# Performance work log

Hardware: AMD Instinct MI355X
Metric: run time of the kernel (lower is better)

The kernel has to match this reference:

```python
import jax, jax.numpy as jnp
import numpy as np

T = 1_048_576          # sequence length
NUM_INPUTS = 16        # symbol vocab for _delta table
MAX_OUTPUT = 25        # softmax width / counter range


def setup_inputs() -> dict:
    key = jax.random.key(0)
    k1, k2, k3 = jax.random.split(key, 3)
    input_seq = jax.random.randint(k1, (T,), 0, NUM_INPUTS)
    # learned params (random instead of the degenerate zero init so the
    # recurrence and softmax are non-trivial)
    delta = jax.random.normal(k2, (NUM_INPUTS,), dtype=jnp.float32) * 0.5
    out_bias = jax.random.normal(k3, (MAX_OUTPUT,), dtype=jnp.float32) * 0.1
    out_scale = jnp.ones((1,), dtype=jnp.float32)
    return {"input_seq": input_seq, "delta": delta,
            "out_bias": out_bias, "out_scale": out_scale}


def reference(input_seq, delta, out_bias, out_scale):
    max_out = out_bias.shape[0]
    # per-step increments: vectorized gather  [T]
    deltas = delta[input_seq]

    # scalar counter recurrence with clamp (non-associative -> lax.scan)
    def step(c, d):
        c = jnp.clip(c + d, 0.0, float(max_out - 1))
        return c, c

    _, counters = jax.lax.scan(step, jnp.float32(0.0), deltas)  # [T]

    # vectorized readout: distances [T, max_out] -> logits -> softmax
    positions = jnp.arange(max_out, dtype=jnp.float32)
    distances = jnp.abs(positions[None, :] - counters[:, None])
    logits = -distances * out_scale + out_bias
    return jax.nn.softmax(logits, axis=-1)  # [T, max_out]
```

## Files before the change

kernel.cpp:

```cpp
#include <hip/hip_runtime.h>

#define T_LEN   1048576
#define K1B     1024
#define BLK     256
#define SEG     256
#define NSEG    (T_LEN / SEG)
#define MAXO    25
#define CLAMP_HI 24.0f
#define BIGF    1e30f

typedef float f4v __attribute__((ext_vector_type(4)));

struct Trip { float a, l, h; };

__device__ __forceinline__ Trip comb(Trip x, Trip y) {
    Trip r;
    r.a = x.a + y.a;
    r.l = fmaxf(x.l + y.a, y.l);
    r.h = fminf(fmaxf(x.h + y.a, y.l), y.h);
    return r;
}
__device__ __forceinline__ float applyT(Trip p, float c) {
    return fminf(fmaxf(c + p.a, p.l), p.h);
}
__device__ __forceinline__ Trip shflUpTrip(Trip v, int off) {
    Trip r;
    r.a = __shfl_up(v.a, off, 64);
    r.l = __shfl_up(v.l, off, 64);
    r.h = __shfl_up(v.h, off, 64);
    return r;
}

__global__ __launch_bounds__(BLK)
void k1_fused(const int* __restrict__ seq, const float* __restrict__ delta,
              float* __restrict__ tri, float* __restrict__ entry,
              int* __restrict__ cnt) {
    __shared__ float dl[16];
    __shared__ int isLast;
    __shared__ Trip agg[4];
    const int tid = threadIdx.x, lane = tid & 63, wid = tid >> 6;
    const int bid = blockIdx.x;

    if (tid < 16) dl[tid] = delta[tid];
    __syncthreads();

    const int4 s4 = *(const int4*)(seq + bid * 1024 + tid * 4);
    Trip t = {dl[s4.x], 0.0f, CLAMP_HI};
    { Trip e = {dl[s4.y], 0.0f, CLAMP_HI}; t = comb(t, e); }
    { Trip e = {dl[s4.z], 0.0f, CLAMP_HI}; t = comb(t, e); }
    { Trip e = {dl[s4.w], 0.0f, CLAMP_HI}; t = comb(t, e); }

#pragma unroll
    for (int off = 1; off < 64; off <<= 1) {
        Trip o = shflUpTrip(t, off);
        if (lane >= off) t = comb(o, t);
    }
    if (lane == 63) {
        const int sid = bid * 4 + wid;
        tri[3 * sid + 0] = t.a;
        tri[3 * sid + 1] = t.l;
        tri[3 * sid + 2] = t.h;
    }
    __syncthreads();
    if (tid == 0) {
        __threadfence();
        isLast = (atomicAdd(cnt, 1) == K1B - 1);
    }
    __syncthreads();
    if (!isLast) return;

    __threadfence();
    f4v f[12];
    const f4v* p = (const f4v*)(tri + tid * 48);
#pragma unroll
    for (int i = 0; i < 12; ++i) f[i] = p[i];
    const float* fp = (const float*)f;

    Trip loc[16];
#pragma unroll
    for (int k = 0; k < 16; ++k)
        loc[k] = {fp[3 * k], fp[3 * k + 1], fp[3 * k + 2]};

    Trip incl = loc[0];
#pragma unroll
    for (int k = 1; k < 16; ++k) incl = comb(incl, loc[k]);

#pragma unroll
    for (int off = 1; off < 64; off <<= 1) {
        Trip o = shflUpTrip(incl, off);
        if (lane >= off) incl = comb(o, incl);
    }
    if (lane == 63) agg[wid] = incl;
    __syncthreads();

    Trip W = {0.0f, -BIGF, BIGF};
    for (int w = 0; w < wid; ++w) W = comb(W, agg[w]);
    const Trip prev = shflUpTrip(incl, 1);
    const Trip E = (lane == 0) ? W : comb(W, prev);

    float ebuf[16];
    float c = applyT(E, 0.0f);
    ebuf[0] = c;
#pragma unroll
    for (int k = 0; k < 15; ++k) { c = applyT(loc[k], c); ebuf[k + 1] = c; }

    f4v* ep = (f4v*)(entry + 16 * tid);
#pragma unroll
    for (int i = 0; i < 4; ++i)
        ep[i] = ((const f4v*)ebuf)[i];
}

__global__ __launch_bounds__(BLK)
void k2_out(const int* __restrict__ seq, const float* __restrict__ delta,
            const float* __restrict__ bias, const float* __restrict__ scale,
            const float* __restrict__ entry, float* __restrict__ out) {
    __shared__ __align__(16) float tile[SEG * MAXO];
    __shared__ Trip agg[4];
    __shared__ float dl[16], bs[MAXO];

    const int tid = threadIdx.x, lane = tid & 63, wid = tid >> 6;
    const int bid = blockIdx.x;

    if (tid < 16)   dl[tid] = delta[tid];
    if (tid < MAXO) bs[tid] = bias[tid];
    const float sfac = scale[0];
    const float cseg = entry[bid];
    const int s = seq[bid * SEG + tid];
    __syncthreads();

    Trip t = {dl[s], 0.0f, CLAMP_HI};
#pragma unroll
    for (int off = 1; off < 64; off <<= 1) {
        Trip o = shflUpTrip(t, off);
        if (lane >= off) t = comb(o, t);
    }
    if (lane == 63) agg[wid] = t;
    __syncthreads();

    float cb = cseg;
    for (int w = 0; w < wid; ++w) cb = applyT(agg[w], cb);
    const float c = applyT(t, cb);

    float ev[MAXO];
    float sum = 0.0f;
#pragma unroll
    for (int j = 0; j < MAXO; ++j) {
        ev[j] = __expf(fmaf(-sfac, fabsf((float)j - c), bs[j]));
        sum += ev[j];
    }
    const float r = 1.0f / sum;
#pragma unroll
    for (int j = 0; j < MAXO; ++j)
        tile[tid * MAXO + j] = ev[j] * r;
    __syncthreads();

    const f4v* tp = (const f4v*)tile;
    f4v* op = (f4v*)(out + (size_t)bid * SEG * MAXO);
#pragma unroll 4
    for (int i = tid; i < SEG * MAXO / 4; i += BLK)
        __builtin_nontemporal_store(tp[i], op + i);
}

extern "C" void kernel_launch(void* const* d_in, const int* in_sizes, int n_in,
                              void* d_out, int out_size, void* d_ws, size_t ws_size,
                              hipStream_t stream) {
    const int*   seq   = (const int*)d_in[0];
    const float* delta = (const float*)d_in[1];
    const float* bias  = (const float*)d_in[2];
    const float* scale = (const float*)d_in[3];
    float* out = (float*)d_out;

    float* tri   = (float*)d_ws;
    float* entry = tri + NSEG * 3;
    int*   cnt   = (int*)(entry + NSEG);

    hipMemsetAsync(cnt, 0, sizeof(int), stream);

    k1_fused<<<K1B, BLK, 0, stream>>>(seq, delta, tri, entry, cnt);
    k2_out  <<<NSEG, BLK, 0, stream>>>(seq, delta, bias, scale, entry, out);
}
```

Measured before the change: 148.8 us.

## Move top-level segment scan into output kernel, drop last-block atomic and memset

```diff
diff --git a/kernel.cpp b/kernel.cpp
--- a/kernel.cpp
+++ b/kernel.cpp
@@ -32,19 +32,15 @@
 }
 
 __global__ __launch_bounds__(BLK)
-void k1_fused(const int* __restrict__ seq, const float* __restrict__ delta,
-              float* __restrict__ tri, float* __restrict__ entry,
-              int* __restrict__ cnt) {
+void k1_seg(const int* __restrict__ seq, const float* __restrict__ delta,
+            float* __restrict__ tri) {
     __shared__ float dl[16];
-    __shared__ int isLast;
-    __shared__ Trip agg[4];
     const int tid = threadIdx.x, lane = tid & 63, wid = tid >> 6;
-    const int bid = blockIdx.x;
 
     if (tid < 16) dl[tid] = delta[tid];
     __syncthreads();
 
-    const int4 s4 = *(const int4*)(seq + bid * 1024 + tid * 4);
+    const int4 s4 = *(const int4*)(seq + blockIdx.x * 1024 + tid * 4);
     Trip t = {dl[s4.x], 0.0f, CLAMP_HI};
     { Trip e = {dl[s4.y], 0.0f, CLAMP_HI}; t = comb(t, e); }
     { Trip e = {dl[s4.z], 0.0f, CLAMP_HI}; t = comb(t, e); }
@@ -56,20 +52,30 @@
         if (lane >= off) t = comb(o, t);
     }
     if (lane == 63) {
-        const int sid = bid * 4 + wid;
+        const int sid = blockIdx.x * 4 + wid;
         tri[3 * sid + 0] = t.a;
         tri[3 * sid + 1] = t.l;
         tri[3 * sid + 2] = t.h;
     }
-    __syncthreads();
-    if (tid == 0) {
-        __threadfence();
-        isLast = (atomicAdd(cnt, 1) == K1B - 1);
-    }
-    __syncthreads();
-    if (!isLast) return;
+}
 
-    __threadfence();
+__global__ __launch_bounds__(BLK)
+void k2_out(const int* __restrict__ seq, const float* __restrict__ delta,
+            const float* __restrict__ bias, const float* __restrict__ scale,
+            const float* __restrict__ tri, float* __restrict__ out) {
+    __shared__ __align__(16) float tile[SEG * MAXO];
+    __shared__ Trip agg[4];
+    __shared__ float dl[16], bs[MAXO];
+    __shared__ float centry;
+
+    const int tid = threadIdx.x, lane = tid & 63, wid = tid >> 6;
+    const int bid = blockIdx.x;
+
+    if (tid < 16)   dl[tid] = delta[tid];
+    if (tid < MAXO) bs[tid] = bias[tid];
+    const float sfac = scale[0];
+    const int s = seq[bid * SEG + tid];
+
     f4v f[12];
     const f4v* p = (const f4v*)(tri + tid * 48);
 #pragma unroll
@@ -98,34 +104,14 @@
     const Trip prev = shflUpTrip(incl, 1);
     const Trip E = (lane == 0) ? W : comb(W, prev);
 
-    float ebuf[16];
-    float c = applyT(E, 0.0f);
-    ebuf[0] = c;
-#pragma unroll
-    for (int k = 0; k < 15; ++k) { c = applyT(loc[k], c); ebuf[k + 1] = c; }
-
-    f4v* ep = (f4v*)(entry + 16 * tid);
-#pragma unroll
-    for (int i = 0; i < 4; ++i)
-        ep[i] = ((const f4v*)ebuf)[i];
-}
-
-__global__ __launch_bounds__(BLK)
-void k2_out(const int* __restrict__ seq, const float* __restrict__ delta,
-            const float* __restrict__ bias, const float* __restrict__ scale,
-            const float* __restrict__ entry, float* __restrict__ out) {
-    __shared__ __align__(16) float tile[SEG * MAXO];
-    __shared__ Trip agg[4];
-    __shared__ float dl[16], bs[MAXO];
-
-    const int tid = threadIdx.x, lane = tid & 63, wid = tid >> 6;
-    const int bid = blockIdx.x;
-
-    if (tid < 16)   dl[tid] = delta[tid];
-    if (tid < MAXO) bs[tid] = bias[tid];
-    const float sfac = scale[0];
-    const float cseg = entry[bid];
-    const int s = seq[bid * SEG + tid];
+    {
+        const int q = bid >> 4, r = bid & 15;
+        if (tid == q) {
+            float c = applyT(E, 0.0f);
+            for (int j = 0; j < r; ++j) c = applyT(loc[j], c);
+            centry = c;
+        }
+    }
     __syncthreads();
 
     Trip t = {dl[s], 0.0f, CLAMP_HI};
@@ -137,7 +123,7 @@
     if (lane == 63) agg[wid] = t;
     __syncthreads();
 
-    float cb = cseg;
+    float cb = centry;
     for (int w = 0; w < wid; ++w) cb = applyT(agg[w], cb);
     const float c = applyT(t, cb);
 
@@ -156,9 +142,9 @@
 
     const f4v* tp = (const f4v*)tile;
     f4v* op = (f4v*)(out + (size_t)bid * SEG * MAXO);
-#pragma unroll 4
+#pragma unroll
     for (int i = tid; i < SEG * MAXO / 4; i += BLK)
-        __builtin_nontemporal_store(tp[i], op + i);
+        op[i] = tp[i];
 }
 
 extern "C" void kernel_launch(void* const* d_in, const int* in_sizes, int n_in,
@@ -170,12 +156,8 @@
     const float* scale = (const float*)d_in[3];
     float* out = (float*)d_out;
 
-    float* tri   = (float*)d_ws;
-    float* entry = tri + NSEG * 3;
-    int*   cnt   = (int*)(entry + NSEG);
+    float* tri = (float*)d_ws;
 
-    hipMemsetAsync(cnt, 0, sizeof(int), stream);
-
-    k1_fused<<<K1B, BLK, 0, stream>>>(seq, delta, tri, entry, cnt);
-    k2_out  <<<NSEG, BLK, 0, stream>>>(seq, delta, bias, scale, entry, out);
+    k1_seg<<<K1B, BLK, 0, stream>>>(seq, delta, tri);
+    k2_out<<<NSEG, BLK, 0, stream>>>(seq, delta, bias, scale, tri, out);
 }
```

Result: slower. 158.1 us (+6.2%).
